# Performance work log

Hardware: AMD Instinct MI355X
Metric: run time of the kernel (lower is better)

## Reference

```python
import jax, jax.numpy as jnp
import numpy as np

L, H, D, F = 4, 8, 64, 256  # layers, heads, head_dim, FAVOR feature dims (n_dims=256 in source)
DM = H * D                   # d_model = 512
EPS = 1e-6                   # fast_transformers LinearAttention eps


def _ln(x, g, b):
    m = jnp.mean(x, -1, keepdims=True)
    v = jnp.mean((x - m) ** 2, -1, keepdims=True)
    return (x - m) * jax.lax.rsqrt(v + 1e-5) * g + b


def _favor(x, omega):
    # FAVOR+ softmax-kernel feature map. x: [B,S,H,D], omega: [D, F//2]
    x = x * (D ** -0.25)  # x * sqrt(softmax_temp), softmax_temp = 1/sqrt(D)
    u = jnp.einsum('bshd,df->bshf', x, omega)
    h = jnp.sum(x * x, -1, keepdims=True) * 0.5
    return jnp.concatenate([jnp.exp(u - h), jnp.exp(-u - h)], -1) * (F ** -0.5)


def _forward(x, pos, enc_w1, enc_b1, enc_w2, enc_b2, enc_g, enc_b,
             wq, bq, wk, bk, wv, bv, wo, bo, ln1_g, ln1_b,
             w1, b1, w2, b2, ln2_g, ln2_b, omega, cls_w, cls_b, num_graphs):
    B = num_graphs
    N = x.shape[0]
    S = N // B
    # encoder MLP + LayerNorm
    h = jnp.concatenate([x, pos], axis=1)
    h = jax.nn.relu(h @ enc_w1 + enc_b1)
    h = _ln(h @ enc_w2 + enc_b2, enc_g, enc_b)
    h = h.reshape(B, S, DM)
    # fast_transformers post-norm encoder layers with linear (FAVOR) attention
    for l in range(L):
        q = (h @ wq[l] + bq[l]).reshape(B, S, H, D)
        k = (h @ wk[l] + bk[l]).reshape(B, S, H, D)
        v = (h @ wv[l] + bv[l]).reshape(B, S, H, D)
        Q = _favor(q, omega[l])  # [B,S,H,F]
        K = _favor(k, omega[l])
        kv = jnp.einsum('bshf,bshd->bhfd', K, v)                      # associative accumulation
        z = 1.0 / (jnp.einsum('bshf,bhf->bsh', Q, K.sum(axis=1)) + EPS)
        a = jnp.einsum('bshf,bhfd,bsh->bshd', Q, kv, z).reshape(B, S, DM)
        h = _ln(h + a @ wo[l] + bo[l], ln1_g[l], ln1_b[l])            # x = norm1(x + attn)
        y = jax.nn.relu(h @ w1[l] + b1[l]) @ w2[l] + b2[l]            # FFN (relu)
        h = _ln(h + y, ln2_g[l], ln2_b[l])                            # norm2(x + y)
    pooled = h.mean(axis=1)
    return pooled @ cls_w + cls_b


def setup_inputs() -> dict:
    key = jax.random.key(0)
    ks = jax.random.split(key, 16)
    B, S = 16, 1024
    N = B * S

    def w(k, shape):
        return jax.random.normal(k, shape, jnp.float32) * 0.02

    return dict(
        x=jax.random.normal(ks[0], (N, 3), jnp.float32),
        pos=jax.random.normal(ks[1], (N, 3), jnp.float32),
        enc_w1=w(ks[2], (6, DM // 2)), enc_b1=jnp.zeros((DM // 2,), jnp.float32),
        enc_w2=w(ks[3], (DM // 2, DM)), enc_b2=jnp.zeros((DM,), jnp.float32),
        enc_g=jnp.ones((DM,), jnp.float32), enc_b=jnp.zeros((DM,), jnp.float32),
        wq=w(ks[4], (L, DM, DM)), bq=jnp.zeros((L, DM), jnp.float32),
        wk=w(ks[5], (L, DM, DM)), bk=jnp.zeros((L, DM), jnp.float32),
        wv=w(ks[6], (L, DM, DM)), bv=jnp.zeros((L, DM), jnp.float32),
        wo=w(ks[7], (L, DM, DM)), bo=jnp.zeros((L, DM), jnp.float32),
        ln1_g=jnp.ones((L, DM), jnp.float32), ln1_b=jnp.zeros((L, DM), jnp.float32),
        w1=w(ks[8], (L, DM, 2 * DM)), b1=jnp.zeros((L, 2 * DM), jnp.float32),
        w2=w(ks[9], (L, 2 * DM, DM)), b2=jnp.zeros((L, DM), jnp.float32),
        ln2_g=jnp.ones((L, DM), jnp.float32), ln2_b=jnp.zeros((L, DM), jnp.float32),
        omega=jax.random.normal(ks[10], (L, D, F // 2), jnp.float32),
        cls_w=w(ks[11], (DM, 16)), cls_b=jnp.zeros((16,), jnp.float32),
        num_graphs=B,
    )


def reference(x, pos, enc_w1, enc_b1, enc_w2, enc_b2, enc_g, enc_b,
              wq, bq, wk, bk, wv, bv, wo, bo, ln1_g, ln1_b,
              w1, b1, w2, b2, ln2_g, ln2_b, omega, cls_w, cls_b, num_graphs):
    return _forward(x, pos, enc_w1, enc_b1, enc_w2, enc_b2, enc_g, enc_b,
                    wq, bq, wk, bk, wv, bv, wo, bo, ln1_g, ln1_b,
                    w1, b1, w2, b2, ln2_g, ln2_b, omega, cls_w, cls_b, num_graphs)
```

## Files before the change

kernel.cpp:

```cpp
#include <hip/hip_runtime.h>
#include <hip/hip_bf16.h>
#include <math.h>

#define NTOK 16384
#define BATCH 16
#define SEQ 1024
#define DMODEL 512
#define NHEAD 8
#define HDIM 64
#define FDIM 256
#define BH_TOT 128
#define SCALE_QK 0.3535533905932738f
#define SCALE2 0.125f
#define FSCALE 0.0625f

typedef __bf16 bf16x8_t __attribute__((ext_vector_type(8)));
typedef float f32x4_t  __attribute__((ext_vector_type(4)));
typedef unsigned short u16x8 __attribute__((ext_vector_type(8)));
typedef unsigned short u16x4 __attribute__((ext_vector_type(4)));
typedef const __attribute__((address_space(1))) char* gas_t;
typedef __attribute__((address_space(3))) char* las_t;

__device__ __forceinline__ float b2f(unsigned short u) {
    union { unsigned int i; float f; } c; c.i = ((unsigned int)u) << 16; return c.f;
}
__device__ __forceinline__ unsigned short f2bu(float f) {
    __hip_bfloat16 h = __float2bfloat16(f);
    return *(unsigned short*)&h;
}
__device__ __forceinline__ bf16x8_t u2b8(u16x8 u) {
    union { u16x8 a; bf16x8_t b; } c; c.a = u; return c.b;
}

__global__ __launch_bounds__(256) void convT_batch_kernel(
    const float* __restrict__ W, unsigned short* __restrict__ Wt, int K, int N,
    size_t in_lstride, size_t out_lstride)
{
    int l = blockIdx.z;
    W  += (size_t)l * in_lstride;
    Wt += (size_t)l * out_lstride;
    __shared__ float tile[32][33];
    int k0 = blockIdx.y * 32, n0 = blockIdx.x * 32;
    int t = threadIdx.x;
    int r = t >> 3, c4 = (t & 7) * 4;
    float4 v = *(const float4*)(W + (size_t)(k0 + r) * N + n0 + c4);
    tile[r][c4 + 0] = v.x; tile[r][c4 + 1] = v.y;
    tile[r][c4 + 2] = v.z; tile[r][c4 + 3] = v.w;
    __syncthreads();
    ushort4 o;
    o.x = f2bu(tile[c4 + 0][r]); o.y = f2bu(tile[c4 + 1][r]);
    o.z = f2bu(tile[c4 + 2][r]); o.w = f2bu(tile[c4 + 3][r]);
    *(ushort4*)(Wt + (size_t)(n0 + r) * K + k0 + c4) = o;
}

__global__ __launch_bounds__(256) void omT_kernel(
    const float* __restrict__ om, unsigned short* __restrict__ omT)
{
    int i = blockIdx.x * 256 + threadIdx.x;
    int l = i >> 13, rem = i & 8191;
    int f = rem >> 6, d = rem & 63;
    omT[(size_t)l * 8192 + f * 64 + d] = f2bu(om[(size_t)l * 8192 + d * 128 + f] * SCALE_QK);
}

__global__ __launch_bounds__(256) void enc1_kernel(
    const float* __restrict__ x, const float* __restrict__ pos,
    const float* __restrict__ w1, const float* __restrict__ b1,
    unsigned short* __restrict__ mid)
{
    int t = threadIdx.x;
    int row0 = blockIdx.x * 8;
    float w[6];
#pragma unroll
    for (int j = 0; j < 6; j++) w[j] = w1[j * 256 + t];
    float bias = b1[t];
#pragma unroll
    for (int rr = 0; rr < 8; rr++) {
        int row = row0 + rr;
        float acc = bias
            + x[row * 3 + 0] * w[0] + x[row * 3 + 1] * w[1] + x[row * 3 + 2] * w[2]
            + pos[row * 3 + 0] * w[3] + pos[row * 3 + 1] * w[4] + pos[row * 3 + 2] * w[5];
        mid[(size_t)row * 256 + t] = f2bu(fmaxf(acc, 0.f));
    }
}

template<int RELU>
__global__ __launch_bounds__(256) void gemm_bf16_kernel(
    const unsigned short* __restrict__ A, const unsigned short* __restrict__ Bt,
    const float* __restrict__ bias, unsigned short* __restrict__ C,
    int M, int K, int Nc, int nx)
{
    __shared__ __align__(16) unsigned short As[128 * 32];
    __shared__ __align__(16) unsigned short Bs[128 * 32];
    const int tid = threadIdx.x;
    const int id = blockIdx.x;
    const int xcd = id & 7, slot = id >> 3;
    const int bm = ((slot / nx) * 8 + xcd) * 128;
    const int bn = (slot % nx) * 128;
    const int wave = tid >> 6, lane = tid & 63;
    const int wr = (wave >> 1) * 64, wc = (wave & 1) * 64;
    const int lm = lane & 15, lk = (lane >> 4) * 8;

    f32x4_t acc[4][4];
#pragma unroll
    for (int i = 0; i < 4; i++)
#pragma unroll
        for (int j = 0; j < 4; j++)
            acc[i][j] = (f32x4_t){0.f, 0.f, 0.f, 0.f};

    for (int k0 = 0; k0 < K; k0 += 32) {
#pragma unroll
        for (int it = 0; it < 2; ++it) {
            int t = tid + it * 256;
            const unsigned short* gp = A + (size_t)(bm + (t >> 2)) * K + k0 + (t & 3) * 8;
            __builtin_amdgcn_global_load_lds((gas_t)(const char*)gp,
                (las_t)((char*)As + t * 16), 16, 0, 0);
        }
#pragma unroll
        for (int it = 0; it < 2; ++it) {
            int t = tid + it * 256;
            const unsigned short* gp = Bt + (size_t)(bn + (t >> 2)) * K + k0 + (t & 3) * 8;
            __builtin_amdgcn_global_load_lds((gas_t)(const char*)gp,
                (las_t)((char*)Bs + t * 16), 16, 0, 0);
        }
        __syncthreads();
        bf16x8_t af[4], bfr[4];
#pragma unroll
        for (int i = 0; i < 4; i++)
            af[i] = *(const bf16x8_t*)(As + (size_t)(wr + 16 * i + lm) * 32 + lk);
#pragma unroll
        for (int j = 0; j < 4; j++)
            bfr[j] = *(const bf16x8_t*)(Bs + (size_t)(wc + 16 * j + lm) * 32 + lk);
#pragma unroll
        for (int i = 0; i < 4; i++)
#pragma unroll
            for (int j = 0; j < 4; j++)
                acc[i][j] = __builtin_amdgcn_mfma_f32_16x16x32_bf16(af[i], bfr[j], acc[i][j], 0, 0, 0);
        __syncthreads();
    }

    const int col_l = lane & 15;
    const int row_q = (lane >> 4) * 4;
#pragma unroll
    for (int i = 0; i < 4; i++) {
#pragma unroll
        for (int j = 0; j < 4; j++) {
            int gn = bn + wc + 16 * j + col_l;
            float bsv = bias[gn];
            int gm0 = bm + wr + 16 * i + row_q;
#pragma unroll
            for (int r = 0; r < 4; r++) {
                float v = acc[i][j][r] + bsv;
                if (RELU) v = fmaxf(v, 0.f);
                C[(size_t)(gm0 + r) * Nc + gn] = f2bu(v);
            }
        }
    }
}

__global__ __launch_bounds__(256) void gemm_qkv_kernel(
    const unsigned short* __restrict__ A, const unsigned short* __restrict__ Bt,
    const float* __restrict__ bq, const float* __restrict__ bk, const float* __restrict__ bv,
    unsigned short* __restrict__ Q, unsigned short* __restrict__ Kk,
    unsigned short* __restrict__ vT)
{
    __shared__ __align__(16) unsigned short As[128 * 32];
    __shared__ __align__(16) unsigned short Bs[128 * 32];
    const int tid = threadIdx.x;
    const int id = blockIdx.x;
    const int xcd = id & 7, slot = id >> 3;
    const int bm = ((slot / 12) * 8 + xcd) * 128;
    const int bn = (slot % 12) * 128;
    const int wave = tid >> 6, lane = tid & 63;
    const int wr = (wave >> 1) * 64, wc = (wave & 1) * 64;
    const int lm = lane & 15, lk = (lane >> 4) * 8;
    const int K = DMODEL;

    f32x4_t acc[4][4];
#pragma unroll
    for (int i = 0; i < 4; i++)
#pragma unroll
        for (int j = 0; j < 4; j++)
            acc[i][j] = (f32x4_t){0.f, 0.f, 0.f, 0.f};

    for (int k0 = 0; k0 < K; k0 += 32) {
#pragma unroll
        for (int it = 0; it < 2; ++it) {
            int t = tid + it * 256;
            const unsigned short* gp = A + (size_t)(bm + (t >> 2)) * K + k0 + (t & 3) * 8;
            __builtin_amdgcn_global_load_lds((gas_t)(const char*)gp,
                (las_t)((char*)As + t * 16), 16, 0, 0);
        }
#pragma unroll
        for (int it = 0; it < 2; ++it) {
            int t = tid + it * 256;
            const unsigned short* gp = Bt + (size_t)(bn + (t >> 2)) * K + k0 + (t & 3) * 8;
            __builtin_amdgcn_global_load_lds((gas_t)(const char*)gp,
                (las_t)((char*)Bs + t * 16), 16, 0, 0);
        }
        __syncthreads();
        bf16x8_t af[4], bfr[4];
#pragma unroll
        for (int i = 0; i < 4; i++)
            af[i] = *(const bf16x8_t*)(As + (size_t)(wr + 16 * i + lm) * 32 + lk);
#pragma unroll
        for (int j = 0; j < 4; j++)
            bfr[j] = *(const bf16x8_t*)(Bs + (size_t)(wc + 16 * j + lm) * 32 + lk);
#pragma unroll
        for (int i = 0; i < 4; i++)
#pragma unroll
            for (int j = 0; j < 4; j++)
                acc[i][j] = __builtin_amdgcn_mfma_f32_16x16x32_bf16(af[i], bfr[j], acc[i][j], 0, 0, 0);
        __syncthreads();
    }

    const int sect = bn >> 9;
    const float* bias = (sect == 0) ? bq : (sect == 1) ? bk : bv;
    unsigned short* rowout = (sect == 0) ? Q : Kk;
    const int cb = bn & 511;
    const int col_l = lane & 15;
    const int row_q = (lane >> 4) * 4;
#pragma unroll
    for (int i = 0; i < 4; i++) {
#pragma unroll
        for (int j = 0; j < 4; j++) {
            int cn = cb + wc + 16 * j + col_l;
            float bsv = bias[cn];
            int gm0 = bm + wr + 16 * i + row_q;
            if (sect < 2) {
#pragma unroll
                for (int r = 0; r < 4; r++)
                    rowout[(size_t)(gm0 + r) * DMODEL + cn] = f2bu(acc[i][j][r] + bsv);
            } else {
                int bb_ = gm0 >> 10, ss = gm0 & 1023;
                int hh_ = cn >> 6, dd = cn & 63;
                u16x4 o4;
#pragma unroll
                for (int r = 0; r < 4; r++) o4[r] = f2bu(acc[i][j][r] + bsv);
                *(u16x4*)(vT + (((size_t)(bb_ * NHEAD + hh_) * HDIM + dd) * SEQ + ss)) = o4;
            }
        }
    }
}

__global__ __launch_bounds__(256) void favor_k_kv_kernel(
    const unsigned short* __restrict__ Kx,
    const unsigned short* __restrict__ vT,
    const unsigned short* __restrict__ omT,
    unsigned short* __restrict__ kvpart,
    float* __restrict__ kspart)
{
    const int bid = blockIdx.x;
    const int xcd = bid & 7, slot = bid >> 3;
    const int chunk = slot & 3;
    const int bh = (slot >> 2) * 8 + xcd;
    const int b = bh >> 3, h = bh & 7;
    const int tid = threadIdx.x;
    const int wave = tid >> 6, lane = tid & 63;
    const int lm = lane & 15, q = lane >> 4, lk = q * 8;
    const int quad4 = q * 4;
    const int wr = wave * 64;
    const int m0 = wave * 16;

    __shared__ __align__(16) unsigned short phiT[256 * 72];

    f32x4_t acc_kv[4][4];
#pragma unroll
    for (int i = 0; i < 4; i++)
#pragma unroll
        for (int j = 0; j < 4; j++)
            acc_kv[i][j] = (f32x4_t){0.f, 0.f, 0.f, 0.f};
    float ks_acc = 0.f;

    const unsigned short* vbase = vT + (size_t)bh * HDIM * SEQ;

    for (int st = 0; st < 4; ++st) {
        int s0 = chunk * 256 + st * 64;
        const unsigned short* krow = Kx + (size_t)(b * SEQ + s0 + m0 + lm) * DMODEL + h * HDIM;
        u16x8 xu0 = *(const u16x8*)(krow + lk);
        u16x8 xu1 = *(const u16x8*)(krow + 32 + lk);
        float p = 0.f;
#pragma unroll
        for (int e = 0; e < 8; e++) {
            float a = b2f(xu0[e]), c = b2f(xu1[e]);
            p += a * a + c * c;
        }
        p += __shfl_xor(p, 16, 64);
        p += __shfl_xor(p, 32, 64);
        float hred = 0.5f * SCALE2 * p;
        float hr[4];
#pragma unroll
        for (int r = 0; r < 4; r++) hr[r] = __shfl(hred, quad4 + r, 64);
        f32x4_t acc[8];
#pragma unroll
        for (int j = 0; j < 8; j++) acc[j] = (f32x4_t){0.f, 0.f, 0.f, 0.f};
        bf16x8_t af0 = u2b8(xu0), af1 = u2b8(xu1);
#pragma unroll
        for (int j = 0; j < 8; j++) {
            bf16x8_t b0 = *(const bf16x8_t*)(omT + (size_t)(j * 16 + lm) * 64 + lk);
            acc[j] = __builtin_amdgcn_mfma_f32_16x16x32_bf16(af0, b0, acc[j], 0, 0, 0);
            bf16x8_t b1 = *(const bf16x8_t*)(omT + (size_t)(j * 16 + lm) * 64 + 32 + lk);
            acc[j] = __builtin_amdgcn_mfma_f32_16x16x32_bf16(af1, b1, acc[j], 0, 0, 0);
        }
        __syncthreads();
#pragma unroll
        for (int j = 0; j < 8; j++) {
            int f = j * 16 + lm;
#pragma unroll
            for (int r = 0; r < 4; r++) {
                int m = m0 + quad4 + r;
                float u = acc[j][r];
                phiT[f * 72 + m]         = f2bu(__expf(u - hr[r]) * FSCALE);
                phiT[(f + 128) * 72 + m] = f2bu(__expf(-u - hr[r]) * FSCALE);
            }
        }
        __syncthreads();
        {
            const unsigned short* row = &phiT[tid * 72];
#pragma unroll
            for (int mm = 0; mm < 64; mm += 8) {
                u16x8 v = *(const u16x8*)(row + mm);
#pragma unroll
                for (int e = 0; e < 8; e++) ks_acc += b2f(v[e]);
            }
        }
#pragma unroll
        for (int ks = 0; ks < 2; ks++) {
            bf16x8_t af[4], bfr[4];
#pragma unroll
            for (int i = 0; i < 4; i++)
                af[i] = *(const bf16x8_t*)&phiT[(wr + 16 * i + lm) * 72 + ks * 32 + lk];
#pragma unroll
            for (int j = 0; j < 4; j++)
                bfr[j] = *(const bf16x8_t*)(vbase + (size_t)(16 * j + lm) * SEQ + s0 + ks * 32 + lk);
#pragma unroll
            for (int i = 0; i < 4; i++)
#pragma unroll
                for (int j = 0; j < 4; j++)
                    acc_kv[i][j] = __builtin_amdgcn_mfma_f32_16x16x32_bf16(af[i], bfr[j], acc_kv[i][j], 0, 0, 0);
        }
    }

    unsigned short* kp = kvpart + ((size_t)chunk * BH_TOT + bh) * HDIM * FDIM;
#pragma unroll
    for (int i = 0; i < 4; i++) {
#pragma unroll
        for (int j = 0; j < 4; j++) {
            int d = 16 * j + lm;
            int f0 = wr + 16 * i + quad4;
            u16x4 o4;
#pragma unroll
            for (int r = 0; r < 4; r++) o4[r] = f2bu(acc_kv[i][j][r]);
            *(u16x4*)(kp + (size_t)d * FDIM + f0) = o4;
        }
    }
    kspart[(size_t)chunk * (BH_TOT * FDIM) + (size_t)bh * FDIM + tid] = ks_acc;
}

__global__ __launch_bounds__(256) void reduce_kv_kernel(
    const unsigned short* __restrict__ in_kv, const float* __restrict__ in_ks,
    unsigned short* __restrict__ out_kv, float* __restrict__ out_ks)
{
    const int NKV = BH_TOT * HDIM * FDIM;
    const int NKS = BH_TOT * FDIM;
    int blk = blockIdx.x;
    if (blk < 1024) {
        size_t base = ((size_t)blk * 256 + threadIdx.x) * 8;
        u16x8 v0 = *(const u16x8*)(in_kv + base);
        u16x8 v1 = *(const u16x8*)(in_kv + base + NKV);
        u16x8 v2 = *(const u16x8*)(in_kv + base + 2 * (size_t)NKV);
        u16x8 v3 = *(const u16x8*)(in_kv + base + 3 * (size_t)NKV);
        u16x8 o;
#pragma unroll
        for (int e = 0; e < 8; e++)
            o[e] = f2bu(b2f(v0[e]) + b2f(v1[e]) + b2f(v2[e]) + b2f(v3[e]));
        *(u16x8*)(out_kv + base) = o;
    } else {
        size_t j = ((size_t)(blk - 1024) * 256 + threadIdx.x) * 4;
        float4 a0 = *(const float4*)(in_ks + j);
        float4 a1 = *(const float4*)(in_ks + j + NKS);
        float4 a2 = *(const float4*)(in_ks + j + 2 * (size_t)NKS);
        float4 a3 = *(const float4*)(in_ks + j + 3 * (size_t)NKS);
        float4 o = make_float4(a0.x + a1.x + a2.x + a3.x, a0.y + a1.y + a2.y + a3.y,
                               a0.z + a1.z + a2.z + a3.z, a0.w + a1.w + a2.w + a3.w);
        *(float4*)(out_ks + j) = o;
    }
}

__global__ __launch_bounds__(256) void favor_q_attn_kernel(
    const unsigned short* __restrict__ Qx,
    const unsigned short* __restrict__ omT,
    const unsigned short* __restrict__ kvT,
    const float* __restrict__ ksum,
    unsigned short* __restrict__ outX)
{
    const int bid = blockIdx.x;
    const int xcd = bid & 7, slot = bid >> 3;
    const int sc = slot & 15;
    const int bh = (slot >> 4) * 8 + xcd;
    const int b = bh >> 3, h = bh & 7;
    const int s0 = sc * 64;
    const int tid = threadIdx.x;
    const int wave = tid >> 6, lane = tid & 63;
    const int lm = lane & 15, q = lane >> 4, lk = q * 8;
    const int quad4 = q * 4;
    const int m0 = wave * 16;

    __shared__ __align__(16) unsigned short phis[4][16 * 136];
    __shared__ __align__(16) float kss[4][256];

    *(float4*)&kss[wave][lane * 4] = *(const float4*)(ksum + (size_t)bh * FDIM + lane * 4);

    const unsigned short* qrow = Qx + (size_t)(b * SEQ + s0 + m0 + lm) * DMODEL + h * HDIM;
    u16x8 xu0 = *(const u16x8*)(qrow + lk);
    u16x8 xu1 = *(const u16x8*)(qrow + 32 + lk);
    float p = 0.f;
#pragma unroll
    for (int e = 0; e < 8; e++) {
        float a = b2f(xu0[e]), c = b2f(xu1[e]);
        p += a * a + c * c;
    }
    p += __shfl_xor(p, 16, 64);
    p += __shfl_xor(p, 32, 64);
    float hred = 0.5f * SCALE2 * p;
    float hr[4];
#pragma unroll
    for (int r = 0; r < 4; r++) hr[r] = __shfl(hred, quad4 + r, 64);

    f32x4_t acc[8];
#pragma unroll
    for (int j = 0; j < 8; j++) acc[j] = (f32x4_t){0.f, 0.f, 0.f, 0.f};
    bf16x8_t af0 = u2b8(xu0), af1 = u2b8(xu1);
#pragma unroll
    for (int j = 0; j < 8; j++) {
        bf16x8_t b0 = *(const bf16x8_t*)(omT + (size_t)(j * 16 + lm) * 64 + lk);
        acc[j] = __builtin_amdgcn_mfma_f32_16x16x32_bf16(af0, b0, acc[j], 0, 0, 0);
        bf16x8_t b1 = *(const bf16x8_t*)(omT + (size_t)(j * 16 + lm) * 64 + 32 + lk);
        acc[j] = __builtin_amdgcn_mfma_f32_16x16x32_bf16(af1, b1, acc[j], 0, 0, 0);
    }

    unsigned short* ph = phis[wave];
    float zp[4] = {0.f, 0.f, 0.f, 0.f};
#pragma unroll
    for (int j = 0; j < 8; j++) {
        int f = j * 16 + lm;
        float ksp = kss[wave][f], ksm = kss[wave][128 + f];
#pragma unroll
        for (int r = 0; r < 4; r++) {
            float u = acc[j][r];
            float pp = __expf(u - hr[r]) * FSCALE;
            float pm = __expf(-u - hr[r]) * FSCALE;
            ph[(quad4 + r) * 136 + f] = f2bu(pp);
            zp[r] += pp * ksp + pm * ksm;
        }
    }
#pragma unroll
    for (int off = 1; off < 16; off <<= 1) {
        zp[0] += __shfl_xor(zp[0], off, 64);
        zp[1] += __shfl_xor(zp[1], off, 64);
        zp[2] += __shfl_xor(zp[2], off, 64);
        zp[3] += __shfl_xor(zp[3], off, 64);
    }
    float zinv[4];
#pragma unroll
    for (int r = 0; r < 4; r++) zinv[r] = 1.f / (zp[r] + 1e-6f);

    const unsigned short* kvbase = kvT + (size_t)bh * HDIM * FDIM;
    f32x4_t acc_o[4];
#pragma unroll
    for (int j = 0; j < 4; j++) acc_o[j] = (f32x4_t){0.f, 0.f, 0.f, 0.f};
#pragma unroll
    for (int k0 = 0; k0 < 128; k0 += 32) {
        bf16x8_t af = *(const bf16x8_t*)&ph[lm * 136 + k0 + lk];
#pragma unroll
        for (int j = 0; j < 4; j++) {
            bf16x8_t bfr = *(const bf16x8_t*)(kvbase + (size_t)(16 * j + lm) * FDIM + k0 + lk);
            acc_o[j] = __builtin_amdgcn_mfma_f32_16x16x32_bf16(af, bfr, acc_o[j], 0, 0, 0);
        }
    }
#pragma unroll
    for (int j = 0; j < 8; j++) {
        int f = j * 16 + lm;
#pragma unroll
        for (int r = 0; r < 4; r++)
            ph[(quad4 + r) * 136 + f] = f2bu(__expf(-acc[j][r] - hr[r]) * FSCALE);
    }
#pragma unroll
    for (int k0 = 0; k0 < 128; k0 += 32) {
        bf16x8_t af = *(const bf16x8_t*)&ph[lm * 136 + k0 + lk];
#pragma unroll
        for (int j = 0; j < 4; j++) {
            bf16x8_t bfr = *(const bf16x8_t*)(kvbase + (size_t)(16 * j + lm) * FDIM + 128 + k0 + lk);
            acc_o[j] = __builtin_amdgcn_mfma_f32_16x16x32_bf16(af, bfr, acc_o[j], 0, 0, 0);
        }
    }
#pragma unroll
    for (int r = 0; r < 4; r++) {
        int s = s0 + m0 + quad4 + r;
#pragma unroll
        for (int j = 0; j < 4; j++) {
            int d = 16 * j + lm;
            outX[(size_t)(b * SEQ + s) * DMODEL + h * HDIM + d] = f2bu(acc_o[j][r] * zinv[r]);
        }
    }
}

template<int HAS_RES>
__global__ __launch_bounds__(512) void add_ln_kernel(
    const unsigned short* __restrict__ res16, const unsigned short* __restrict__ tin16,
    const float* __restrict__ g, const float* __restrict__ bb,
    unsigned short* __restrict__ out16)
{
    int wave = threadIdx.x >> 6, lane = threadIdx.x & 63;
    int row = blockIdx.x * 8 + wave;
    size_t base = (size_t)row * DMODEL + lane * 8;
    u16x8 tv = *(const u16x8*)(tin16 + base);
    float v[8];
    float s1 = 0.f, s2 = 0.f;
    if (HAS_RES) {
        u16x8 rv = *(const u16x8*)(res16 + base);
#pragma unroll
        for (int e = 0; e < 8; e++) v[e] = b2f(tv[e]) + b2f(rv[e]);
    } else {
#pragma unroll
        for (int e = 0; e < 8; e++) v[e] = b2f(tv[e]);
    }
#pragma unroll
    for (int e = 0; e < 8; e++) { s1 += v[e]; s2 += v[e] * v[e]; }
#pragma unroll
    for (int off = 1; off < 64; off <<= 1) {
        s1 += __shfl_xor(s1, off, 64);
        s2 += __shfl_xor(s2, off, 64);
    }
    float m = s1 * (1.f / DMODEL);
    float var = s2 * (1.f / DMODEL) - m * m;
    float r = rsqrtf(var + 1e-5f);
    float4 g0 = *(const float4*)(g + lane * 8);
    float4 g1 = *(const float4*)(g + lane * 8 + 4);
    float4 b0 = *(const float4*)(bb + lane * 8);
    float4 b1 = *(const float4*)(bb + lane * 8 + 4);
    float gg[8] = {g0.x, g0.y, g0.z, g0.w, g1.x, g1.y, g1.z, g1.w};
    float bbv[8] = {b0.x, b0.y, b0.z, b0.w, b1.x, b1.y, b1.z, b1.w};
    u16x8 o;
#pragma unroll
    for (int e = 0; e < 8; e++)
        o[e] = f2bu((v[e] - m) * r * gg[e] + bbv[e]);
    *(u16x8*)(out16 + base) = o;
}

__global__ __launch_bounds__(256) void pool_part_kernel(
    const unsigned short* __restrict__ h16, float* __restrict__ pbuf)
{
    int blk = blockIdx.x;
    int b = blk >> 4, ch = blk & 15;
    int t = threadIdx.x;
    int d0 = t * 2;
    float a0 = 0.f, a1 = 0.f;
    const unsigned short* base = h16 + ((size_t)(b * SEQ + ch * 64) * DMODEL) + d0;
#pragma unroll 4
    for (int s = 0; s < 64; s++) {
        ushort2 v = *(const ushort2*)(base + (size_t)s * DMODEL);
        a0 += b2f(v.x); a1 += b2f(v.y);
    }
    *(float2*)(pbuf + (size_t)blk * DMODEL + d0) = make_float2(a0, a1);
}

__global__ __launch_bounds__(512) void cls_kernel(
    const float* __restrict__ pbuf, const float* __restrict__ cls_w,
    const float* __restrict__ cls_b, float* __restrict__ out)
{
    int b = blockIdx.x, t = threadIdx.x;
    float s = 0.f;
#pragma unroll
    for (int c = 0; c < 16; c++) s += pbuf[(size_t)(b * 16 + c) * DMODEL + t];
    __shared__ float pooled[DMODEL];
    pooled[t] = s * (1.f / SEQ);
    __syncthreads();
    if (t < 16) {
        float acc = cls_b[t];
        for (int c = 0; c < DMODEL; c++) acc += pooled[c] * cls_w[c * 16 + t];
        out[b * 16 + t] = acc;
    }
}

extern "C" void kernel_launch(void* const* d_in, const int* in_sizes, int n_in,
                              void* d_out, int out_size, void* d_ws, size_t ws_size,
                              hipStream_t stream)
{
    const float* x      = (const float*)d_in[0];
    const float* pos    = (const float*)d_in[1];
    const float* enc_w1 = (const float*)d_in[2];
    const float* enc_b1 = (const float*)d_in[3];
    const float* enc_w2 = (const float*)d_in[4];
    const float* enc_b2 = (const float*)d_in[5];
    const float* enc_g  = (const float*)d_in[6];
    const float* enc_bb = (const float*)d_in[7];
    const float* wq = (const float*)d_in[8];
    const float* bq = (const float*)d_in[9];
    const float* wk = (const float*)d_in[10];
    const float* bk = (const float*)d_in[11];
    const float* wv = (const float*)d_in[12];
    const float* bv = (const float*)d_in[13];
    const float* wo = (const float*)d_in[14];
    const float* bo = (const float*)d_in[15];
    const float* ln1_g = (const float*)d_in[16];
    const float* ln1_b = (const float*)d_in[17];
    const float* w1 = (const float*)d_in[18];
    const float* b1 = (const float*)d_in[19];
    const float* w2 = (const float*)d_in[20];
    const float* b2 = (const float*)d_in[21];
    const float* ln2_g = (const float*)d_in[22];
    const float* ln2_b = (const float*)d_in[23];
    const float* omega = (const float*)d_in[24];
    const float* cls_w = (const float*)d_in[25];
    const float* cls_b = (const float*)d_in[26];
    float* out = (float*)d_out;

    const int N = NTOK;
    const int BH = BH_TOT;

    char* p = (char*)d_ws;
    unsigned short* qb16 = (unsigned short*)p; p += (size_t)N * DMODEL * 2;
    unsigned short* kb16 = (unsigned short*)p; p += (size_t)N * DMODEL * 2;
    unsigned short* vT16 = (unsigned short*)p; p += (size_t)N * DMODEL * 2;
    unsigned short* h16  = (unsigned short*)p; p += (size_t)N * DMODEL * 2;
    unsigned short* mid16 = (unsigned short*)p; p += (size_t)N * 1024 * 2;
    unsigned short* attn16 = (unsigned short*)p; p += (size_t)N * DMODEL * 2;
    unsigned short* kvpart = (unsigned short*)p; p += (size_t)4 * BH * HDIM * FDIM * 2;
    float* kspart = (float*)p;                 p += (size_t)4 * BH * FDIM * 4;
    unsigned short* kvT16 = (unsigned short*)p; p += (size_t)BH * HDIM * FDIM * 2;
    float* ksb = (float*)p;                    p += (size_t)BH * FDIM * 4;
    float* pbuf = (float*)p;                   p += (size_t)BATCH * 16 * DMODEL * 4;
    unsigned short* enc_w2t = (unsigned short*)p; p += (size_t)256 * 512 * 2;
    unsigned short* wqkvt = (unsigned short*)p; p += (size_t)4 * 1536 * 512 * 2;
    unsigned short* wot = (unsigned short*)p;  p += (size_t)4 * 512 * 512 * 2;
    unsigned short* w1t = (unsigned short*)p;  p += (size_t)4 * 512 * 1024 * 2;
    unsigned short* w2t = (unsigned short*)p;  p += (size_t)4 * 1024 * 512 * 2;
    unsigned short* omT = (unsigned short*)p;  p += (size_t)4 * 128 * 64 * 2;

    convT_batch_kernel<<<dim3(16, 8, 1), 256, 0, stream>>>(enc_w2, enc_w2t, 256, 512, 0, 0);
    convT_batch_kernel<<<dim3(16, 16, 4), 256, 0, stream>>>(wq, wqkvt,            512, 512, 262144, 786432);
    convT_batch_kernel<<<dim3(16, 16, 4), 256, 0, stream>>>(wk, wqkvt + 262144,   512, 512, 262144, 786432);
    convT_batch_kernel<<<dim3(16, 16, 4), 256, 0, stream>>>(wv, wqkvt + 524288,   512, 512, 262144, 786432);
    convT_batch_kernel<<<dim3(16, 16, 4), 256, 0, stream>>>(wo, wot, 512, 512, 262144, 262144);
    convT_batch_kernel<<<dim3(32, 16, 4), 256, 0, stream>>>(w1, w1t, 512, 1024, 524288, 524288);
    convT_batch_kernel<<<dim3(16, 32, 4), 256, 0, stream>>>(w2, w2t, 1024, 512, 524288, 524288);
    omT_kernel<<<128, 256, 0, stream>>>(omega, omT);

    enc1_kernel<<<N / 8, 256, 0, stream>>>(x, pos, enc_w1, enc_b1, mid16);
    gemm_bf16_kernel<0><<<4 * 128, 256, 0, stream>>>(mid16, enc_w2t, enc_b2, qb16, N, 256, 512, 4);
    add_ln_kernel<0><<<N / 8, 512, 0, stream>>>(nullptr, qb16, enc_g, enc_bb, h16);

    for (int l = 0; l < 4; l++) {
        const unsigned short* omT_l = omT + (size_t)l * 8192;
        gemm_qkv_kernel<<<12 * 128, 256, 0, stream>>>(
            h16, wqkvt + (size_t)l * 786432,
            bq + l * DMODEL, bk + l * DMODEL, bv + l * DMODEL,
            qb16, kb16, vT16);
        favor_k_kv_kernel<<<BH * 4, 256, 0, stream>>>(kb16, vT16, omT_l, kvpart, kspart);
        reduce_kv_kernel<<<1056, 256, 0, stream>>>(kvpart, kspart, kvT16, ksb);
        favor_q_attn_kernel<<<BH * 16, 256, 0, stream>>>(qb16, omT_l, kvT16, ksb, attn16);
        gemm_bf16_kernel<0><<<4 * 128, 256, 0, stream>>>(attn16, wot + (size_t)l * 262144, bo + l * DMODEL, qb16, N, 512, 512, 4);
        add_ln_kernel<1><<<N / 8, 512, 0, stream>>>(h16, qb16, ln1_g + l * DMODEL, ln1_b + l * DMODEL, h16);
        gemm_bf16_kernel<1><<<8 * 128, 256, 0, stream>>>(h16, w1t + (size_t)l * 524288, b1 + l * 1024, mid16, N, 512, 1024, 8);
        gemm_bf16_kernel<0><<<4 * 128, 256, 0, stream>>>(mid16, w2t + (size_t)l * 524288, b2 + l * DMODEL, qb16, N, 1024, 512, 4);
        add_ln_kernel<1><<<N / 8, 512, 0, stream>>>(h16, qb16, ln2_g + l * DMODEL, ln2_b + l * DMODEL, h16);
    }

    pool_part_kernel<<<BATCH * 16, 256, 0, stream>>>(h16, pbuf);
    cls_kernel<<<BATCH, 512, 0, stream>>>(pbuf, cls_w, cls_b, out);
}
```

Before: 1.045 ms.

## Fuse output GEMMs with residual LayerNorm and retile FAVOR query attention

Adds a GEMM kernel that computes a full 32x512 output row block per workgroup and applies bias, residual add and LayerNorm in the epilogue. This replaces the separate gemm plus add_ln pairs for the encoder, attention output and FFN down projections. It removes the bf16 intermediate round trip and nine launches. The trade-off is a tall-skinny tile with 32 rows that reloads the full 512-column weight slice for every block, and it has no double buffering. The FAVOR query kernel also moves to 128-thread blocks covering 32 rows, writes the positive and negative features at the same time, and merges the two kv MFMA loops into one.

```diff
diff --git a/kernel.cpp b/kernel.cpp
--- a/kernel.cpp
+++ b/kernel.cpp
@@ -157,6 +157,121 @@
     }
 }
 
+template<int HAS_RES>
+__global__ __launch_bounds__(256) void gemm_ln_kernel(
+    const unsigned short* __restrict__ A,
+    const unsigned short* __restrict__ Bt,
+    const float* __restrict__ bias,
+    const unsigned short* __restrict__ res16,
+    const float* __restrict__ g, const float* __restrict__ bb,
+    unsigned short* __restrict__ out,
+    int K)
+{
+    __shared__ __align__(16) unsigned short As[32 * 32];
+    __shared__ __align__(16) unsigned short Bs[512 * 32];
+    __shared__ float part[4][32][2];
+    const int tid = threadIdx.x;
+    const int bm = blockIdx.x * 32;
+    const int wave = tid >> 6, lane = tid & 63;
+    const int wc = wave * 128;
+    const int lm = lane & 15, q = lane >> 4, lk = q * 8;
+    const int quad4 = q * 4;
+
+    f32x4_t acc[2][8];
+#pragma unroll
+    for (int i = 0; i < 2; i++)
+#pragma unroll
+        for (int j = 0; j < 8; j++)
+            acc[i][j] = (f32x4_t){0.f, 0.f, 0.f, 0.f};
+
+    for (int k0 = 0; k0 < K; k0 += 32) {
+        if (tid < 128) {
+            const unsigned short* gp = A + (size_t)(bm + (tid >> 2)) * K + k0 + (tid & 3) * 8;
+            __builtin_amdgcn_global_load_lds((gas_t)(const char*)gp,
+                (las_t)((char*)As + tid * 16), 16, 0, 0);
+        }
+#pragma unroll
+        for (int it = 0; it < 8; ++it) {
+            int t = tid + it * 256;
+            const unsigned short* gp = Bt + (size_t)(t >> 2) * K + k0 + (t & 3) * 8;
+            __builtin_amdgcn_global_load_lds((gas_t)(const char*)gp,
+                (las_t)((char*)Bs + t * 16), 16, 0, 0);
+        }
+        __syncthreads();
+        bf16x8_t af[2], bfr[8];
+#pragma unroll
+        for (int i = 0; i < 2; i++)
+            af[i] = *(const bf16x8_t*)(As + (size_t)(16 * i + lm) * 32 + lk);
+#pragma unroll
+        for (int j = 0; j < 8; j++)
+            bfr[j] = *(const bf16x8_t*)(Bs + (size_t)(wc + 16 * j + lm) * 32 + lk);
+#pragma unroll
+        for (int i = 0; i < 2; i++)
+#pragma unroll
+            for (int j = 0; j < 8; j++)
+                acc[i][j] = __builtin_amdgcn_mfma_f32_16x16x32_bf16(af[i], bfr[j], acc[i][j], 0, 0, 0);
+        __syncthreads();
+    }
+
+    float s1[2][4] = {}, s2[2][4] = {};
+#pragma unroll
+    for (int i = 0; i < 2; i++) {
+#pragma unroll
+        for (int j = 0; j < 8; j++) {
+            int col = wc + 16 * j + lm;
+            float bsv = bias[col];
+#pragma unroll
+            for (int r = 0; r < 4; r++) {
+                float v = acc[i][j][r] + bsv;
+                if (HAS_RES)
+                    v += b2f(res16[(size_t)(bm + 16 * i + quad4 + r) * DMODEL + col]);
+                acc[i][j][r] = v;
+                s1[i][r] += v;
+                s2[i][r] += v * v;
+            }
+        }
+    }
+#pragma unroll
+    for (int off = 1; off < 16; off <<= 1) {
+#pragma unroll
+        for (int i = 0; i < 2; i++)
+#pragma unroll
+            for (int r = 0; r < 4; r++) {
+                s1[i][r] += __shfl_xor(s1[i][r], off, 64);
+                s2[i][r] += __shfl_xor(s2[i][r], off, 64);
+            }
+    }
+    if (lm == 0) {
+#pragma unroll
+        for (int i = 0; i < 2; i++)
+#pragma unroll
+            for (int r = 0; r < 4; r++) {
+                int rl = 16 * i + quad4 + r;
+                part[wave][rl][0] = s1[i][r];
+                part[wave][rl][1] = s2[i][r];
+            }
+    }
+    __syncthreads();
+#pragma unroll
+    for (int i = 0; i < 2; i++) {
+#pragma unroll
+        for (int r = 0; r < 4; r++) {
+            int rl = 16 * i + quad4 + r;
+            float t1 = part[0][rl][0] + part[1][rl][0] + part[2][rl][0] + part[3][rl][0];
+            float t2 = part[0][rl][1] + part[1][rl][1] + part[2][rl][1] + part[3][rl][1];
+            float mean = t1 * (1.f / DMODEL);
+            float var = t2 * (1.f / DMODEL) - mean * mean;
+            float rstd = rsqrtf(var + 1e-5f);
+#pragma unroll
+            for (int j = 0; j < 8; j++) {
+                int col = wc + 16 * j + lm;
+                float o = (acc[i][j][r] - mean) * rstd * g[col] + bb[col];
+                out[(size_t)(bm + rl) * DMODEL + col] = f2bu(o);
+            }
+        }
+    }
+}
+
 __global__ __launch_bounds__(256) void gemm_qkv_kernel(
     const unsigned short* __restrict__ A, const unsigned short* __restrict__ Bt,
     const float* __restrict__ bq, const float* __restrict__ bk, const float* __restrict__ bv,
@@ -386,7 +501,7 @@
     }
 }
 
-__global__ __launch_bounds__(256) void favor_q_attn_kernel(
+__global__ __launch_bounds__(128) void favor_q_attn_kernel(
     const unsigned short* __restrict__ Qx,
     const unsigned short* __restrict__ omT,
     const unsigned short* __restrict__ kvT,
@@ -395,18 +510,18 @@
 {
     const int bid = blockIdx.x;
     const int xcd = bid & 7, slot = bid >> 3;
-    const int sc = slot & 15;
-    const int bh = (slot >> 4) * 8 + xcd;
+    const int sc = slot & 31;
+    const int bh = (slot >> 5) * 8 + xcd;
     const int b = bh >> 3, h = bh & 7;
-    const int s0 = sc * 64;
+    const int s0 = sc * 32;
     const int tid = threadIdx.x;
     const int wave = tid >> 6, lane = tid & 63;
     const int lm = lane & 15, q = lane >> 4, lk = q * 8;
     const int quad4 = q * 4;
     const int m0 = wave * 16;
 
-    __shared__ __align__(16) unsigned short phis[4][16 * 136];
-    __shared__ __align__(16) float kss[4][256];
+    __shared__ __align__(16) unsigned short phis[2][2][16 * 136];
+    __shared__ __align__(16) float kss[2][256];
 
     *(float4*)&kss[wave][lane * 4] = *(const float4*)(ksum + (size_t)bh * FDIM + lane * 4);
 
@@ -438,7 +553,8 @@
         acc[j] = __builtin_amdgcn_mfma_f32_16x16x32_bf16(af1, b1, acc[j], 0, 0, 0);
     }
 
-    unsigned short* ph = phis[wave];
+    unsigned short* ph0 = phis[wave][0];
+    unsigned short* ph1 = phis[wave][1];
     float zp[4] = {0.f, 0.f, 0.f, 0.f};
 #pragma unroll
     for (int j = 0; j < 8; j++) {
@@ -449,7 +565,8 @@
             float u = acc[j][r];
             float pp = __expf(u - hr[r]) * FSCALE;
             float pm = __expf(-u - hr[r]) * FSCALE;
-            ph[(quad4 + r) * 136 + f] = f2bu(pp);
+            ph0[(quad4 + r) * 136 + f] = f2bu(pp);
+            ph1[(quad4 + r) * 136 + f] = f2bu(pm);
             zp[r] += pp * ksp + pm * ksm;
         }
     }
@@ -470,27 +587,14 @@
     for (int j = 0; j < 4; j++) acc_o[j] = (f32x4_t){0.f, 0.f, 0.f, 0.f};
 #pragma unroll
     for (int k0 = 0; k0 < 128; k0 += 32) {
-        bf16x8_t af = *(const bf16x8_t*)&ph[lm * 136 + k0 + lk];
+        bf16x8_t a0 = *(const bf16x8_t*)&ph0[lm * 136 + k0 + lk];
+        bf16x8_t a1 = *(const bf16x8_t*)&ph1[lm * 136 + k0 + lk];
 #pragma unroll
         for (int j = 0; j < 4; j++) {
-            bf16x8_t bfr = *(const bf16x8_t*)(kvbase + (size_t)(16 * j + lm) * FDIM + k0 + lk);
-            acc_o[j] = __builtin_amdgcn_mfma_f32_16x16x32_bf16(af, bfr, acc_o[j], 0, 0, 0);
-        }
-    }
-#pragma unroll
-    for (int j = 0; j < 8; j++) {
-        int f = j * 16 + lm;
-#pragma unroll
-        for (int r = 0; r < 4; r++)
-            ph[(quad4 + r) * 136 + f] = f2bu(__expf(-acc[j][r] - hr[r]) * FSCALE);
-    }
-#pragma unroll
-    for (int k0 = 0; k0 < 128; k0 += 32) {
-        bf16x8_t af = *(const bf16x8_t*)&ph[lm * 136 + k0 + lk];
-#pragma unroll
-        for (int j = 0; j < 4; j++) {
-            bf16x8_t bfr = *(const bf16x8_t*)(kvbase + (size_t)(16 * j + lm) * FDIM + 128 + k0 + lk);
-            acc_o[j] = __builtin_amdgcn_mfma_f32_16x16x32_bf16(af, bfr, acc_o[j], 0, 0, 0);
+            bf16x8_t b0 = *(const bf16x8_t*)(kvbase + (size_t)(16 * j + lm) * FDIM + k0 + lk);
+            acc_o[j] = __builtin_amdgcn_mfma_f32_16x16x32_bf16(a0, b0, acc_o[j], 0, 0, 0);
+            bf16x8_t b1 = *(const bf16x8_t*)(kvbase + (size_t)(16 * j + lm) * FDIM + 128 + k0 + lk);
+            acc_o[j] = __builtin_amdgcn_mfma_f32_16x16x32_bf16(a1, b1, acc_o[j], 0, 0, 0);
         }
     }
 #pragma unroll
@@ -502,49 +606,6 @@
             outX[(size_t)(b * SEQ + s) * DMODEL + h * HDIM + d] = f2bu(acc_o[j][r] * zinv[r]);
         }
     }
-}
-
-template<int HAS_RES>
-__global__ __launch_bounds__(512) void add_ln_kernel(
-    const unsigned short* __restrict__ res16, const unsigned short* __restrict__ tin16,
-    const float* __restrict__ g, const float* __restrict__ bb,
-    unsigned short* __restrict__ out16)
-{
-    int wave = threadIdx.x >> 6, lane = threadIdx.x & 63;
-    int row = blockIdx.x * 8 + wave;
-    size_t base = (size_t)row * DMODEL + lane * 8;
-    u16x8 tv = *(const u16x8*)(tin16 + base);
-    float v[8];
-    float s1 = 0.f, s2 = 0.f;
-    if (HAS_RES) {
-        u16x8 rv = *(const u16x8*)(res16 + base);
-#pragma unroll
-        for (int e = 0; e < 8; e++) v[e] = b2f(tv[e]) + b2f(rv[e]);
-    } else {
-#pragma unroll
-        for (int e = 0; e < 8; e++) v[e] = b2f(tv[e]);
-    }
-#pragma unroll
-    for (int e = 0; e < 8; e++) { s1 += v[e]; s2 += v[e] * v[e]; }
-#pragma unroll
-    for (int off = 1; off < 64; off <<= 1) {
-        s1 += __shfl_xor(s1, off, 64);
-        s2 += __shfl_xor(s2, off, 64);
-    }
-    float m = s1 * (1.f / DMODEL);
-    float var = s2 * (1.f / DMODEL) - m * m;
-    float r = rsqrtf(var + 1e-5f);
-    float4 g0 = *(const float4*)(g + lane * 8);
-    float4 g1 = *(const float4*)(g + lane * 8 + 4);
-    float4 b0 = *(const float4*)(bb + lane * 8);
-    float4 b1 = *(const float4*)(bb + lane * 8 + 4);
-    float gg[8] = {g0.x, g0.y, g0.z, g0.w, g1.x, g1.y, g1.z, g1.w};
-    float bbv[8] = {b0.x, b0.y, b0.z, b0.w, b1.x, b1.y, b1.z, b1.w};
-    u16x8 o;
-#pragma unroll
-    for (int e = 0; e < 8; e++)
-        o[e] = f2bu((v[e] - m) * r * gg[e] + bbv[e]);
-    *(u16x8*)(out16 + base) = o;
 }
 
 __global__ __launch_bounds__(256) void pool_part_kernel(
@@ -647,8 +708,7 @@
     omT_kernel<<<128, 256, 0, stream>>>(omega, omT);
 
     enc1_kernel<<<N / 8, 256, 0, stream>>>(x, pos, enc_w1, enc_b1, mid16);
-    gemm_bf16_kernel<0><<<4 * 128, 256, 0, stream>>>(mid16, enc_w2t, enc_b2, qb16, N, 256, 512, 4);
-    add_ln_kernel<0><<<N / 8, 512, 0, stream>>>(nullptr, qb16, enc_g, enc_bb, h16);
+    gemm_ln_kernel<0><<<N / 32, 256, 0, stream>>>(mid16, enc_w2t, enc_b2, nullptr, enc_g, enc_bb, h16, 256);
 
     for (int l = 0; l < 4; l++) {
         const unsigned short* omT_l = omT + (size_t)l * 8192;
@@ -658,12 +718,12 @@
             qb16, kb16, vT16);
         favor_k_kv_kernel<<<BH * 4, 256, 0, stream>>>(kb16, vT16, omT_l, kvpart, kspart);
         reduce_kv_kernel<<<1056, 256, 0, stream>>>(kvpart, kspart, kvT16, ksb);
-        favor_q_attn_kernel<<<BH * 16, 256, 0, stream>>>(qb16, omT_l, kvT16, ksb, attn16);
-        gemm_bf16_kernel<0><<<4 * 128, 256, 0, stream>>>(attn16, wot + (size_t)l * 262144, bo + l * DMODEL, qb16, N, 512, 512, 4);
-        add_ln_kernel<1><<<N / 8, 512, 0, stream>>>(h16, qb16, ln1_g + l * DMODEL, ln1_b + l * DMODEL, h16);
+        favor_q_attn_kernel<<<BH * 32, 128, 0, stream>>>(qb16, omT_l, kvT16, ksb, attn16);
+        gemm_ln_kernel<1><<<N / 32, 256, 0, stream>>>(attn16, wot + (size_t)l * 262144,
+            bo + l * DMODEL, h16, ln1_g + l * DMODEL, ln1_b + l * DMODEL, h16, 512);
         gemm_bf16_kernel<1><<<8 * 128, 256, 0, stream>>>(h16, w1t + (size_t)l * 524288, b1 + l * 1024, mid16, N, 512, 1024, 8);
-        gemm_bf16_kernel<0><<<4 * 128, 256, 0, stream>>>(mid16, w2t + (size_t)l * 524288, b2 + l * DMODEL, qb16, N, 1024, 512, 4);
-        add_ln_kernel<1><<<N / 8, 512, 0, stream>>>(h16, qb16, ln2_g + l * DMODEL, ln2_b + l * DMODEL, h16);
+        gemm_ln_kernel<1><<<N / 32, 256, 0, stream>>>(mid16, w2t + (size_t)l * 524288,
+            b2 + l * DMODEL, h16, ln2_g + l * DMODEL, ln2_b + l * DMODEL, h16, 1024);
     }
 
     pool_part_kernel<<<BATCH * 16, 256, 0, stream>>>(h16, pbuf);
```

Measured after the change: 1.102 ms. +5.5%, slower.
